# Optimization experiments

Hardware: AMD Instinct MI355X
Metric: run time of the kernel (lower is better)

## Reference

```python
import jax, jax.numpy as jnp
import numpy as np

DIM_V = 512
NUM_HEADS = 8
LN_EPS = 1e-5


def _layernorm(x):
    # LayerNorm over last dim, no affine (simplified_layer_norm=True)
    mu = jnp.mean(x, axis=-1, keepdims=True)
    var = jnp.mean(jnp.square(x - mu), axis=-1, keepdims=True)
    return (x - mu) * jax.lax.rsqrt(var + LN_EPS)


def setup_inputs() -> dict:
    key = jax.random.key(0)
    ks = jax.random.split(key, 12)
    B, Nq, Nk, dQ, dK, dV = 16, 1024, 1024, 512, 512, DIM_V
    s = 0.02
    return {
        "Q": jax.random.normal(ks[0], (B, Nq, dQ), jnp.float32),
        "K": jax.random.normal(ks[1], (B, Nk, dK), jnp.float32),
        "Wq": jax.random.normal(ks[2], (dQ, dV), jnp.float32) * s,
        "bq": jnp.zeros((dV,), jnp.float32),
        "Wk": jax.random.normal(ks[3], (dK, dV), jnp.float32) * s,
        "bk": jnp.zeros((dV,), jnp.float32),
        "Wv": jax.random.normal(ks[4], (dK, dV), jnp.float32) * s,
        "bv": jnp.zeros((dV,), jnp.float32),
        "Wo": jax.random.normal(ks[5], (dV, dV), jnp.float32) * s,
        "bo": jnp.zeros((dV,), jnp.float32),
    }


def reference(Q, K, Wq, bq, Wk, bk, Wv, bv, Wo, bo):
    H = NUM_HEADS
    dh = DIM_V // H
    q = Q @ Wq + bq            # [B, Nq, dV]
    k = K @ Wk + bk            # [B, Nk, dV]
    v = K @ Wv + bv            # [B, Nk, dV]
    B, Nq, _ = q.shape
    Nk = k.shape[1]
    qh = q.reshape(B, Nq, H, dh)
    kh = k.reshape(B, Nk, H, dh)
    vh = v.reshape(B, Nk, H, dh)
    # NOTE: faithful to source — scale by sqrt(dim_V), not sqrt(head_dim)
    scores = jnp.einsum('bqhd,bkhd->bhqk', qh, kh) / jnp.sqrt(jnp.asarray(DIM_V, q.dtype))
    A = jax.nn.softmax(scores, axis=-1)                    # [B, H, Nq, Nk]
    attn = jnp.einsum('bhqk,bkhd->bqhd', A, vh).reshape(B, Nq, DIM_V)
    O = q + attn               # residual with projected Q
    O = _layernorm(O)          # ln0 (no affine)
    O = O + jax.nn.gelu(O @ Wo + bo, approximate=False)
    O = _layernorm(O)          # ln1 (no affine)
    return O
```

## Files before the change

### kernel.cpp

```cpp
#include <hip/hip_runtime.h>
#include <hip/hip_bf16.h>
#include <math.h>

typedef __bf16 bf16;
typedef __bf16 bf16x8 __attribute__((ext_vector_type(8)));
typedef float  f32x4  __attribute__((ext_vector_type(4)));
typedef float  f32x16 __attribute__((ext_vector_type(16)));
typedef unsigned u32x4 __attribute__((ext_vector_type(4)));

#define MFMA16(a,b,c) __builtin_amdgcn_mfma_f32_16x16x32_bf16((a),(b),(c),0,0,0)
#define MFMA32(a,b,c) __builtin_amdgcn_mfma_f32_32x32x16_bf16((a),(b),(c),0,0,0)
#define KSCALE 0.0637587159f

__device__ __forceinline__ void async16p(const void* g, void* l) {
    __builtin_amdgcn_global_load_lds((const __attribute__((address_space(1))) void*)g,
                                     (__attribute__((address_space(3))) void*)l,
                                     16, 0, 0);
}

__device__ __forceinline__ float fexp2(float x) {
#if __has_builtin(__builtin_amdgcn_exp2f)
    return __builtin_amdgcn_exp2f(x);
#else
    return exp2f(x);
#endif
}

__device__ __forceinline__ unsigned pkbf(float a, float b) {
    union { bf16 h[2]; unsigned u; } x;
    x.h[0] = (bf16)a; x.h[1] = (bf16)b; return x.u;
}

__device__ __forceinline__ void plswap(unsigned &a, unsigned &b) {
#if __has_builtin(__builtin_amdgcn_permlane32_swap)
    auto r = __builtin_amdgcn_permlane32_swap((int)a, (int)b, false, false);
    a = (unsigned)r[0]; b = (unsigned)r[1];
#else
    unsigned sa = (unsigned)__shfl_xor((int)a, 32);
    unsigned sb = (unsigned)__shfl_xor((int)b, 32);
    bool hi = (threadIdx.x & 32) != 0;
    unsigned na = hi ? sb : a;
    unsigned nb = hi ? b  : sa;
    a = na; b = nb;
#endif
}

__global__ __launch_bounds__(256) void prep_w_kernel(
    const float* __restrict__ Wq, const float* __restrict__ Wk,
    const float* __restrict__ Wv, const float* __restrict__ Wo,
    bf16* __restrict__ WqT, bf16* __restrict__ WkT,
    bf16* __restrict__ WvT, bf16* __restrict__ WoT,
    float* __restrict__ csum)
{
    __shared__ float tile[32][33];
    const int bx = blockIdx.x;
    const float* W; bf16* T;
    switch (bx >> 8) {
      case 0: W=Wq; T=WqT; break;
      case 1: W=Wk; T=WkT; break;
      case 2: W=Wv; T=WvT; break;
      default: W=Wo; T=WoT; break;
    }
    const int rest = bx & 255;
    const int k0 = (rest & 15) * 32, n0 = (rest >> 4) * 32;
    const int tx = threadIdx.x & 31, ty = threadIdx.x >> 5;
    float sacc = 0.f;
    #pragma unroll
    for (int i=0;i<32;i+=8) {
        float v = W[(size_t)(k0+ty+i)*512 + n0+tx];
        tile[ty+i][tx] = v;
        sacc += v;
    }
    __syncthreads();
    #pragma unroll
    for (int i=0;i<32;i+=8)
        T[(size_t)(n0+ty+i)*512 + k0+tx] = (bf16)tile[tx][ty+i];
    if ((bx >> 8) == 3) {
        __syncthreads();
        tile[ty][tx] = sacc;
        __syncthreads();
        if (ty == 0) {
            float s = 0.f;
            #pragma unroll
            for (int j=0;j<8;j++) s += tile[j][tx];
            atomicAdd(&csum[n0+tx], s);
        }
    }
}

__global__ __launch_bounds__(256, 2) void gemm_proj_kernel(
    const float* __restrict__ Qf, const float* __restrict__ Kf,
    const bf16* __restrict__ WqT, const bf16* __restrict__ WkT,
    const bf16* __restrict__ WvT,
    const float* __restrict__ bq, const float* __restrict__ bk,
    const float* __restrict__ bv,
    bf16* __restrict__ qbb, bf16* __restrict__ kbb, bf16* __restrict__ vT)
{
    __shared__ __align__(16) char smem[65536];
    float* As32 = (float*)smem;
    bf16*  Bs   = (bf16*)(smem + 32768);
    bf16*  Lt   = (bf16*)smem;

    const int x = blockIdx.x;
    const bool isQ = (x < 256);
    int m0, n0;
    const float* A; const bf16 *BT0, *BT1; const float *bb0, *bb1;
    if (isQ) {
        const int n = (x >> 3) & 1;
        const int m = (x & 7) | ((x >> 4) << 3);
        m0 = m * 128; n0 = n * 128;
        A = Qf; BT0 = WqT + (size_t)n0*512; BT1 = WqT + (size_t)(n0+256)*512;
        bb0 = bq + n0; bb1 = bq + n0 + 256;
    } else {
        const int r = x - 256;
        const int n = (r >> 3) & 3;
        const int m = (r & 7) | ((r >> 5) << 3);
        m0 = m * 128; n0 = n * 128;
        A = Kf; BT0 = WkT + (size_t)n0*512; BT1 = WvT + (size_t)n0*512;
        bb0 = bk + n0; bb1 = bv + n0;
    }

    const int tid = threadIdx.x;
    const int lane = tid & 63, wave = tid >> 6;
    const int qd = lane >> 4, lr = lane & 15;
    const int wm = (wave & 1) * 64, wn = (wave >> 1) * 64;

    const float* gA = A + (size_t)(m0 + (tid>>3))*512 + (((tid&7)^((tid>>3)&7))*4);
    const int bgr = ((tid & 3) ^ ((tid >> 3) & 3)) * 8;
    const bf16* gB0 = BT0 + (size_t)(tid>>2)*512 + bgr;
    const bf16* gB1 = BT1 + (size_t)(tid>>2)*512 + bgr;

    f32x4 acc[2][4][4];
    #pragma unroll
    for (int p=0;p<2;p++)
      #pragma unroll
      for (int i=0;i<4;i++)
        #pragma unroll
        for (int j=0;j<4;j++) acc[p][i][j] = (f32x4){0,0,0,0};

    auto stage = [&](int buf, int k0) {
        float* lA = As32 + buf*4096 + wave*256;
        #pragma unroll
        for (int i=0;i<4;i++)
            async16p(gA + k0 + (size_t)i*32*512, lA + i*1024);
        bf16* lB0 = Bs + buf*8192 + wave*512;
        async16p(gB0 + k0,                  lB0);
        async16p(gB0 + k0 + (size_t)64*512, lB0 + 2048);
        bf16* lB1 = Bs + buf*8192 + 4096 + wave*512;
        async16p(gB1 + k0,                  lB1);
        async16p(gB1 + k0 + (size_t)64*512, lB1 + 2048);
    };

    stage(0, 0);
    for (int t = 0; t < 16; ++t) {
        const int cur = t & 1;
        __builtin_amdgcn_sched_barrier(0);
        __builtin_amdgcn_s_barrier();
        if (t < 15) {
            stage(cur ^ 1, (t+1)*32);
            asm volatile("s_waitcnt vmcnt(8)" ::: "memory");
        } else {
            asm volatile("s_waitcnt vmcnt(0)" ::: "memory");
        }
        __builtin_amdgcn_s_barrier();

        const float* Ab = As32 + cur*4096;
        const bf16*  Bb = Bs   + cur*8192;
        bf16x8 af[4], bfr[2][4];
        #pragma unroll
        for (int mi=0;mi<4;mi++) {
            int row = wm + mi*16 + lr;
            f32x4 f0 = *(f32x4*)(Ab + row*32 + (((qd*2  )^(lr&7))*4));
            f32x4 f1 = *(f32x4*)(Ab + row*32 + (((qd*2+1)^(lr&7))*4));
            bf16x8 a;
            a[0]=(bf16)f0[0]; a[1]=(bf16)f0[1]; a[2]=(bf16)f0[2]; a[3]=(bf16)f0[3];
            a[4]=(bf16)f1[0]; a[5]=(bf16)f1[1]; a[6]=(bf16)f1[2]; a[7]=(bf16)f1[3];
            af[mi] = a;
        }
        #pragma unroll
        for (int p=0;p<2;p++)
          #pragma unroll
          for (int ni=0;ni<4;ni++)
            bfr[p][ni] = *(bf16x8*)(Bb + p*4096 + (wn+ni*16+lr)*32
                                       + ((qd^((lr>>1)&3))*8));
        #pragma unroll
        for (int p=0;p<2;p++)
          #pragma unroll
          for (int mi=0;mi<4;mi++)
            #pragma unroll
            for (int ni=0;ni<4;ni++)
              acc[p][mi][ni] = MFMA16(af[mi], bfr[p][ni], acc[p][mi][ni]);
    }

    if (isQ) {
        #pragma unroll
        for (int p=0;p<2;p++) {
            const float* bb = p ? bb1 : bb0;
            #pragma unroll
            for (int ni=0;ni<4;ni++) {
                int nl = wn + ni*16 + lr;
                int n = n0 + p*256 + nl;
                float bv0 = bb[nl];
                #pragma unroll
                for (int mi=0;mi<4;mi++) {
                    int mb = m0 + wm + mi*16 + qd*4;
                    #pragma unroll
                    for (int r=0;r<4;r++)
                        qbb[(size_t)(mb+r)*512 + n] = (bf16)(acc[p][mi][ni][r] + bv0);
                }
            }
        }
    } else {
        #pragma unroll
        for (int ni=0;ni<4;ni++) {
            int nl = wn + ni*16 + lr;
            int n = n0 + nl;
            float bv0 = bb0[nl];
            #pragma unroll
            for (int mi=0;mi<4;mi++) {
                int mb = m0 + wm + mi*16 + qd*4;
                #pragma unroll
                for (int r=0;r<4;r++)
                    kbb[(size_t)(mb+r)*512 + n] = (bf16)((acc[0][mi][ni][r] + bv0)*KSCALE);
            }
        }
        const int b = m0 >> 10, tok0 = m0 & 1023;
        const int row = tid >> 2, ch = tid & 3;
        #pragma unroll
        for (int half = 0; half < 2; ++half) {
            __syncthreads();
            if ((wn >> 6) == half) {
                #pragma unroll
                for (int ni=0;ni<4;ni++) {
                    int nl = ni*16 + lr;
                    float bvv = bb1[half*64 + nl];
                    #pragma unroll
                    for (int mi=0;mi<4;mi++)
                      #pragma unroll
                      for (int r=0;r<4;r++) {
                        int col = wm + mi*16 + qd*4 + r;
                        Lt[nl*128 + ((((col>>3)^(nl&7))<<3) | (col&7))]
                            = (bf16)(acc[1][mi][ni][r] + bvv);
                      }
                }
            }
            __syncthreads();
            const int h = (n0 >> 6) + half;
            bf16* dst = vT + ((size_t)((b*8 + h)*64 + row))*1024 + tok0 + ch*32;
            #pragma unroll
            for (int s=0;s<4;s++) {
                int g = (ch*4 + s) ^ (row & 7);
                *(uint4*)(dst + s*8) = *(uint4*)(Lt + row*128 + g*8);
            }
        }
    }
}

__global__ __launch_bounds__(256, 4) void attn_kernel(
    const bf16* __restrict__ qb, const bf16* __restrict__ kb,
    const bf16* __restrict__ vT, bf16* __restrict__ attnb)
{
    const int x = blockIdx.x;
    const int qt = x >> 7, h = x & 7, b = (x & 127) >> 3;
    const int tid = threadIdx.x, lane = tid & 63, wave = tid >> 6;
    const int l = lane & 31, hi = lane >> 5;
    const int q0w = qt*128 + wave*32;

    __shared__ __align__(16) bf16 kv[2][2][4096];
    __shared__ float ls[4][32];

    bf16x8 aq[4];
    {
        const bf16* qrow = qb + ((size_t)(b*1024 + q0w + l))*512 + h*64 + hi*8;
        #pragma unroll
        for (int st=0; st<4; ++st) aq[st] = *(const bf16x8*)(qrow + st*16);
    }

    const int srow = lane >> 3;
    const int sgA  = (lane & 7) ^ srow ^ wave;
    const int sgB  = sgA ^ 4;
    const bf16* kg0 = kb + ((size_t)(b*1024 + wave*8 + srow))*512      + h*64 + sgA*8;
    const bf16* kg1 = kb + ((size_t)(b*1024 + wave*8 + srow + 32))*512 + h*64 + sgB*8;
    const bf16* vg0 = vT + ((size_t)((b*8 + h)*64 + wave*8 + srow))*1024      + sgA*8;
    const bf16* vg1 = vT + ((size_t)((b*8 + h)*64 + wave*8 + srow + 32))*1024 + sgB*8;

    auto stage = [&](int buf, int t) {
        const size_t ko = (size_t)t*64*512;
        async16p(kg0 + ko,     &kv[buf][0][wave*512]);
        async16p(kg1 + ko,     &kv[buf][0][2048 + wave*512]);
        async16p(vg0 + t*64,   &kv[buf][1][wave*512]);
        async16p(vg1 + t*64,   &kv[buf][1][2048 + wave*512]);
    };

    f32x16 accO[2];
    accO[0] = (f32x16)0.f; accO[1] = (f32x16)0.f;
    float lsum = 0.f;
    const int kx = (l & 7) ^ (l >> 3);

    stage(0, 0);
    for (int t=0; t<16; ++t) {
        const int cur = t & 1;
        __builtin_amdgcn_sched_barrier(0);
        __builtin_amdgcn_s_barrier();
        if (t < 15) {
            stage(cur ^ 1, t + 1);
            asm volatile("s_waitcnt vmcnt(4)" ::: "memory");
        } else {
            asm volatile("s_waitcnt vmcnt(0)" ::: "memory");
        }
        __builtin_amdgcn_s_barrier();

        const bf16* Ks = kv[cur][0];
        const bf16* Vs = kv[cur][1];

        u32x4 paf[4];
        #pragma unroll
        for (int kb2=0; kb2<2; ++kb2) {
            f32x16 sT = (f32x16)0.f;
            __builtin_amdgcn_s_setprio(1);
            #pragma unroll
            for (int st=0; st<4; ++st) {
                bf16x8 kf = *(const bf16x8*)(Ks + (kb2*32 + l)*64
                               + (((st*2 + hi) ^ kx ^ (kb2<<2))*8));
                sT = MFMA32(kf, aq[st], sT);
            }
            __builtin_amdgcn_s_setprio(0);
            unsigned u[8];
            #pragma unroll
            for (int m=0; m<8; ++m) {
                float e0 = fexp2(sT[2*m]);
                float e1 = fexp2(sT[2*m+1]);
                lsum += e0 + e1;
                u[m] = pkbf(e0, e1);
            }
            #pragma unroll
            for (int sb=0; sb<2; ++sb) {
                unsigned a0=u[4*sb], a1=u[4*sb+1], a2=u[4*sb+2], a3=u[4*sb+3];
                plswap(a0, a2);
                plswap(a1, a3);
                paf[kb2*2 + sb] = (u32x4){a0, a1, a2, a3};
            }
        }
        __builtin_amdgcn_s_setprio(1);
        #pragma unroll
        for (int db=0; db<2; ++db) {
            f32x16 a = accO[db];
            #pragma unroll
            for (int st=0; st<4; ++st) {
                bf16x8 vf = *(const bf16x8*)(Vs + (db*32 + l)*64
                               + (((st*2 + hi) ^ kx ^ (db<<2))*8));
                u32x4 pp = paf[st];
                bf16x8 pf = *(bf16x8*)&pp;
                a = MFMA32(pf, vf, a);
            }
            accO[db] = a;
        }
        __builtin_amdgcn_s_setprio(0);
    }

    lsum += __shfl_xor(lsum, 32);
    ls[wave][l] = lsum;
    __syncthreads();

    #pragma unroll
    for (int g=0; g<4; ++g) {
        f32x4 lv = *(const f32x4*)(&ls[wave][g*8 + hi*4]);
        f32x4 inv;
        #pragma unroll
        for (int i=0;i<4;i++) inv[i] = 1.f / lv[i];
        #pragma unroll
        for (int db=0; db<2; ++db) {
            #pragma unroll
            for (int i=0;i<4;i++) {
                int r = g*4 + i;
                int qrow = q0w + g*8 + hi*4 + i;
                size_t idx = ((size_t)(b*1024 + qrow))*512 + h*64 + db*32 + l;
                float o = accO[db][r] * inv[i] + (float)qb[idx];
                attnb[idx] = (bf16)o;
            }
        }
    }
}

__global__ __launch_bounds__(256, 4) void gemm_o_kernel(
    const bf16* __restrict__ attnb, const bf16* __restrict__ WoT,
    const float* __restrict__ bo, const float* __restrict__ csum,
    bf16* __restrict__ xb)
{
    __shared__ __align__(16) char smem[24576];
    __shared__ float2 rs[64];
    bf16* As = (bf16*)smem;
    bf16* Bs = (bf16*)(smem + 8192);
    const int m0 = blockIdx.x * 64, n0 = blockIdx.y * 128;
    const int tid = threadIdx.x;
    const int lane = tid & 63, wave = tid >> 6;
    const int qd = lane >> 4, lr = lane & 15;
    const int wm = (wave & 1) * 32, wn = (wave >> 1) * 64;

    const int bgr = ((tid & 3) ^ ((tid >> 3) & 3)) * 8;
    const bf16* gA = attnb + (size_t)(m0 + (tid>>2))*512 + bgr;
    const bf16* gB = WoT   + (size_t)(n0 + (tid>>2))*512 + bgr;

    f32x4 acc[2][4];
    #pragma unroll
    for (int i=0;i<2;i++)
      #pragma unroll
      for (int j=0;j<4;j++) acc[i][j] = (f32x4){0,0,0,0};
    float s1[2] = {0.f, 0.f}, s2[2] = {0.f, 0.f};

    auto stage = [&](int buf, int k0) {
        async16p(gA + k0,                  As + buf*2048 + wave*512);
        bf16* lB = Bs + buf*4096 + wave*512;
        async16p(gB + k0,                  lB);
        async16p(gB + k0 + (size_t)64*512, lB + 2048);
    };

    stage(0, 0);
    for (int t = 0; t < 16; ++t) {
        const int cur = t & 1;
        __builtin_amdgcn_sched_barrier(0);
        __builtin_amdgcn_s_barrier();
        if (t < 15) {
            stage(cur ^ 1, (t+1)*32);
            asm volatile("s_waitcnt vmcnt(3)" ::: "memory");
        } else {
            asm volatile("s_waitcnt vmcnt(0)" ::: "memory");
        }
        __builtin_amdgcn_s_barrier();

        const bf16* Ab = As + cur*2048;
        const bf16* Bb = Bs + cur*4096;
        bf16x8 af[2], bfr[4];
        #pragma unroll
        for (int mi=0;mi<2;mi++) {
            af[mi] = *(bf16x8*)(Ab + (wm+mi*16+lr)*32 + ((qd^((lr>>1)&3))*8));
            #pragma unroll
            for (int j=0;j<8;j++) {
                float v = (float)af[mi][j];
                s1[mi] += v;
                s2[mi] += v*v;
            }
        }
        #pragma unroll
        for (int ni=0;ni<4;ni++)
            bfr[ni] = *(bf16x8*)(Bb + (wn+ni*16+lr)*32 + ((qd^((lr>>1)&3))*8));
        #pragma unroll
        for (int mi=0;mi<2;mi++)
          #pragma unroll
          for (int ni=0;ni<4;ni++)
            acc[mi][ni] = MFMA16(af[mi], bfr[ni], acc[mi][ni]);
    }

    #pragma unroll
    for (int mi=0;mi<2;mi++) {
        s1[mi] += __shfl_xor(s1[mi], 16); s2[mi] += __shfl_xor(s2[mi], 16);
        s1[mi] += __shfl_xor(s1[mi], 32); s2[mi] += __shfl_xor(s2[mi], 32);
    }
    if (wave < 2 && qd == 0) {
        #pragma unroll
        for (int mi=0;mi<2;mi++) {
            float mu  = s1[mi] * (1.f/512.f);
            float var = s2[mi] * (1.f/512.f) - mu*mu;
            rs[wm + mi*16 + lr] = make_float2(mu, rsqrtf(var + 1e-5f));
        }
    }
    __syncthreads();

    float csn[4], bon[4];
    #pragma unroll
    for (int ni=0;ni<4;ni++) {
        int n = n0 + wn + ni*16 + lr;
        csn[ni] = csum[n];
        bon[ni] = bo[n];
    }
    #pragma unroll
    for (int mi=0;mi<2;mi++) {
        #pragma unroll
        for (int r=0;r<4;r++) {
            int rl = wm + mi*16 + qd*4 + r;
            int row = m0 + rl;
            float2 st = rs[rl];
            float mu = st.x, rstd = st.y;
            #pragma unroll
            for (int ni=0;ni<4;ni++) {
                int n = n0 + wn + ni*16 + lr;
                float g = rstd*acc[mi][ni][r] - rstd*mu*csn[ni] + bon[ni];
                float gelu = 0.5f * g * (1.f + erff(g * 0.70710678118654752f));
                size_t idx = (size_t)row*512 + n;
                float lnx = ((float)attnb[idx] - mu) * rstd;
                xb[idx] = (bf16)(lnx + gelu);
            }
        }
    }
}

__global__ __launch_bounds__(256) void ln1_kernel(
    const bf16* __restrict__ xb, float* __restrict__ out)
{
    const int wave = threadIdx.x >> 6, lane = threadIdx.x & 63;
    const int row = blockIdx.x*4 + wave;
    const size_t base = (size_t)row*512 + lane*8;
    bf16x8 xv = *(const bf16x8*)(xb + base);
    float x[8];
    #pragma unroll
    for (int i=0;i<8;i++) x[i] = (float)xv[i];
    float s1 = 0.f, s2 = 0.f;
    #pragma unroll
    for (int i=0;i<8;i++){ s1 += x[i]; s2 += x[i]*x[i]; }
    #pragma unroll
    for (int off=1; off<64; off<<=1) { s1 += __shfl_xor(s1, off); s2 += __shfl_xor(s2, off); }
    float mu  = s1 * (1.f/512.f);
    float var = s2 * (1.f/512.f) - mu*mu;
    float rstd = rsqrtf(var + 1e-5f);
    float4 o0 = {(x[0]-mu)*rstd,(x[1]-mu)*rstd,(x[2]-mu)*rstd,(x[3]-mu)*rstd};
    float4 o1 = {(x[4]-mu)*rstd,(x[5]-mu)*rstd,(x[6]-mu)*rstd,(x[7]-mu)*rstd};
    *(float4*)(out + base)     = o0;
    *(float4*)(out + base + 4) = o1;
}

extern "C" void kernel_launch(void* const* d_in, const int* in_sizes, int n_in,
                              void* d_out, int out_size, void* d_ws, size_t ws_size,
                              hipStream_t stream)
{
    (void)in_sizes; (void)n_in; (void)out_size; (void)ws_size;
    const float* Q  = (const float*)d_in[0];
    const float* K  = (const float*)d_in[1];
    const float* Wq = (const float*)d_in[2];
    const float* bq = (const float*)d_in[3];
    const float* Wk = (const float*)d_in[4];
    const float* bk = (const float*)d_in[5];
    const float* Wv = (const float*)d_in[6];
    const float* bv = (const float*)d_in[7];
    const float* Wo = (const float*)d_in[8];
    const float* bo = (const float*)d_in[9];
    float* out = (float*)d_out;

    const size_t nTok = (size_t)16*1024*512;
    char* p = (char*)d_ws;
    auto alloc = [&](size_t bytes)->char* {
        char* r = p; p += (bytes + 255) & ~(size_t)255; return r;
    };
    bf16*   WqT   = (bf16*)alloc(512*512*2);
    bf16*   WkT   = (bf16*)alloc(512*512*2);
    bf16*   WvT   = (bf16*)alloc(512*512*2);
    bf16*   WoT   = (bf16*)alloc(512*512*2);
    bf16*   qbb   = (bf16*)alloc(nTok*2);
    bf16*   kbb   = (bf16*)alloc(nTok*2);
    bf16*   vT    = (bf16*)alloc(nTok*2);
    bf16*   attnb = (bf16*)alloc(nTok*2);
    bf16*   xb    = (bf16*)alloc(nTok*2);
    float*  csum  = (float*)alloc(512*4);

    hipMemsetAsync(csum, 0, 512*sizeof(float), stream);
    prep_w_kernel<<<1024, 256, 0, stream>>>(Wq, Wk, Wv, Wo, WqT, WkT, WvT, WoT, csum);
    gemm_proj_kernel<<<768, 256, 0, stream>>>(Q, K, WqT, WkT, WvT,
                                              bq, bk, bv, qbb, kbb, vT);
    attn_kernel<<<dim3(1024), 256, 0, stream>>>(qbb, kbb, vT, attnb);
    gemm_o_kernel<<<dim3(256,4), 256, 0, stream>>>(attnb, WoT, bo, csum, xb);
    ln1_kernel<<<4096, 256, 0, stream>>>(xb, out);
}
```

Baseline: 243.5 us.

## Convert projection A tile to bf16 in registers before LDS; drop csum atomics

The projection GEMM no longer async-copies fp32 A tiles into LDS and converts them at fragment-load time. It now loads fp32 A into registers two stages ahead, packs it to bf16, and writes a swizzled bf16 tile to LDS. This shrinks LDS from 64KB to 48KB and halves A's LDS read traffic, at the cost of extra registers and explicit waitcnt choreography. Separately, the Wo column-sum atomics and the memset are replaced by per-block partial sums that gemm_o reduces over 16 entries.

```diff
diff --git a/kernel.cpp b/kernel.cpp
--- a/kernel.cpp
+++ b/kernel.cpp
@@ -50,7 +50,7 @@
     const float* __restrict__ Wv, const float* __restrict__ Wo,
     bf16* __restrict__ WqT, bf16* __restrict__ WkT,
     bf16* __restrict__ WvT, bf16* __restrict__ WoT,
-    float* __restrict__ csum)
+    float* __restrict__ csump)
 {
     __shared__ float tile[32][33];
     const int bx = blockIdx.x;
@@ -83,7 +83,7 @@
             float s = 0.f;
             #pragma unroll
             for (int j=0;j<8;j++) s += tile[j][tx];
-            atomicAdd(&csum[n0+tx], s);
+            csump[(rest & 15)*512 + n0 + tx] = s;
         }
     }
 }
@@ -96,10 +96,10 @@
     const float* __restrict__ bv,
     bf16* __restrict__ qbb, bf16* __restrict__ kbb, bf16* __restrict__ vT)
 {
-    __shared__ __align__(16) char smem[65536];
-    float* As32 = (float*)smem;
-    bf16*  Bs   = (bf16*)(smem + 32768);
-    bf16*  Lt   = (bf16*)smem;
+    __shared__ __align__(16) char smem[49152];
+    bf16* Asb = (bf16*)smem;
+    bf16* Bs  = (bf16*)(smem + 16384);
+    bf16* Lt  = (bf16*)smem;
 
     const int x = blockIdx.x;
     const bool isQ = (x < 256);
@@ -125,7 +125,13 @@
     const int qd = lane >> 4, lr = lane & 15;
     const int wm = (wave & 1) * 64, wn = (wave >> 1) * 64;
 
-    const float* gA = A + (size_t)(m0 + (tid>>3))*512 + (((tid&7)^((tid>>3)&7))*4);
+    const int arow = tid >> 1, ahalf = tid & 1;
+    const float* gAr = A + (size_t)(m0 + arow)*512 + ahalf*16;
+    const int akey = (arow >> 1) & 3;
+    const int ap0 = (2*ahalf) ^ akey;
+    const int ap1 = ap0 ^ 1;
+    bf16* awr = Asb + arow*32;
+
     const int bgr = ((tid & 3) ^ ((tid >> 3) & 3)) * 8;
     const bf16* gB0 = BT0 + (size_t)(tid>>2)*512 + bgr;
     const bf16* gB1 = BT1 + (size_t)(tid>>2)*512 + bgr;
@@ -138,11 +144,7 @@
         #pragma unroll
         for (int j=0;j<4;j++) acc[p][i][j] = (f32x4){0,0,0,0};
 
-    auto stage = [&](int buf, int k0) {
-        float* lA = As32 + buf*4096 + wave*256;
-        #pragma unroll
-        for (int i=0;i<4;i++)
-            async16p(gA + k0 + (size_t)i*32*512, lA + i*1024);
+    auto stageB = [&](int buf, int k0) {
         bf16* lB0 = Bs + buf*8192 + wave*512;
         async16p(gB0 + k0,                  lB0);
         async16p(gB0 + k0 + (size_t)64*512, lB0 + 2048);
@@ -150,33 +152,27 @@
         async16p(gB1 + k0,                  lB1);
         async16p(gB1 + k0 + (size_t)64*512, lB1 + 2048);
     };
-
-    stage(0, 0);
-    for (int t = 0; t < 16; ++t) {
-        const int cur = t & 1;
-        __builtin_amdgcn_sched_barrier(0);
-        __builtin_amdgcn_s_barrier();
-        if (t < 15) {
-            stage(cur ^ 1, (t+1)*32);
-            asm volatile("s_waitcnt vmcnt(8)" ::: "memory");
-        } else {
-            asm volatile("s_waitcnt vmcnt(0)" ::: "memory");
-        }
-        __builtin_amdgcn_s_barrier();
-
-        const float* Ab = As32 + cur*4096;
-        const bf16*  Bb = Bs   + cur*8192;
+    auto loadA = [&](f32x4 (&ar)[4], int k0) {
+        ar[0] = *(const f32x4*)(gAr + k0);
+        ar[1] = *(const f32x4*)(gAr + k0 + 4);
+        ar[2] = *(const f32x4*)(gAr + k0 + 8);
+        ar[3] = *(const f32x4*)(gAr + k0 + 12);
+    };
+    auto writeA = [&](f32x4 (&ar)[4], int buf) {
+        u32x4 w0 = { pkbf(ar[0][0],ar[0][1]), pkbf(ar[0][2],ar[0][3]),
+                     pkbf(ar[1][0],ar[1][1]), pkbf(ar[1][2],ar[1][3]) };
+        u32x4 w1 = { pkbf(ar[2][0],ar[2][1]), pkbf(ar[2][2],ar[2][3]),
+                     pkbf(ar[3][0],ar[3][1]), pkbf(ar[3][2],ar[3][3]) };
+        *(u32x4*)(awr + buf*4096 + ap0*8) = w0;
+        *(u32x4*)(awr + buf*4096 + ap1*8) = w1;
+    };
+    auto compute = [&](int cur) {
+        const bf16* Ab = Asb + cur*4096;
+        const bf16* Bb = Bs  + cur*8192;
         bf16x8 af[4], bfr[2][4];
         #pragma unroll
-        for (int mi=0;mi<4;mi++) {
-            int row = wm + mi*16 + lr;
-            f32x4 f0 = *(f32x4*)(Ab + row*32 + (((qd*2  )^(lr&7))*4));
-            f32x4 f1 = *(f32x4*)(Ab + row*32 + (((qd*2+1)^(lr&7))*4));
-            bf16x8 a;
-            a[0]=(bf16)f0[0]; a[1]=(bf16)f0[1]; a[2]=(bf16)f0[2]; a[3]=(bf16)f0[3];
-            a[4]=(bf16)f1[0]; a[5]=(bf16)f1[1]; a[6]=(bf16)f1[2]; a[7]=(bf16)f1[3];
-            af[mi] = a;
-        }
+        for (int mi=0;mi<4;mi++)
+            af[mi] = *(bf16x8*)(Ab + (wm+mi*16+lr)*32 + ((qd ^ ((lr>>1)&3))*8));
         #pragma unroll
         for (int p=0;p<2;p++)
           #pragma unroll
@@ -190,6 +186,47 @@
             #pragma unroll
             for (int ni=0;ni<4;ni++)
               acc[p][mi][ni] = MFMA16(af[mi], bfr[p][ni], acc[p][mi][ni]);
+    };
+
+    f32x4 aR0[4], aR1[4];
+    loadA(aR0, 0);
+    asm volatile("s_waitcnt vmcnt(0)" ::: "memory");
+    writeA(aR0, 0);
+    loadA(aR0, 32);
+    stageB(0, 0);
+    asm volatile("s_waitcnt lgkmcnt(0)" ::: "memory");
+
+    auto phase = [&](int t, f32x4 (&aWr)[4], f32x4 (&aLd)[4]) {
+        __builtin_amdgcn_sched_barrier(0);
+        __builtin_amdgcn_s_barrier();
+        loadA(aLd, (t+2)*32);
+        stageB((t+1)&1, (t+1)*32);
+        asm volatile("s_waitcnt vmcnt(8)" ::: "memory");
+        writeA(aWr, (t+1)&1);
+        asm volatile("s_waitcnt lgkmcnt(0)" ::: "memory");
+        __builtin_amdgcn_s_barrier();
+        compute(t & 1);
+    };
+
+    #pragma unroll 1
+    for (int tt = 0; tt < 7; ++tt) {
+        phase(2*tt,   aR0, aR1);
+        phase(2*tt+1, aR1, aR0);
+    }
+    {
+        __builtin_amdgcn_sched_barrier(0);
+        __builtin_amdgcn_s_barrier();
+        stageB(1, 480);
+        asm volatile("s_waitcnt vmcnt(4)" ::: "memory");
+        writeA(aR0, 1);
+        asm volatile("s_waitcnt lgkmcnt(0)" ::: "memory");
+        __builtin_amdgcn_s_barrier();
+        compute(0);
+    }
+    {
+        asm volatile("s_waitcnt vmcnt(0)" ::: "memory");
+        __builtin_amdgcn_s_barrier();
+        compute(1);
     }
 
     if (isQ) {
@@ -384,7 +421,7 @@
 
 __global__ __launch_bounds__(256, 4) void gemm_o_kernel(
     const bf16* __restrict__ attnb, const bf16* __restrict__ WoT,
-    const float* __restrict__ bo, const float* __restrict__ csum,
+    const float* __restrict__ bo, const float* __restrict__ csump,
     bf16* __restrict__ xb)
 {
     __shared__ __align__(16) char smem[24576];
@@ -470,7 +507,10 @@
     #pragma unroll
     for (int ni=0;ni<4;ni++) {
         int n = n0 + wn + ni*16 + lr;
-        csn[ni] = csum[n];
+        float s = 0.f;
+        #pragma unroll
+        for (int kb=0;kb<16;kb++) s += csump[kb*512 + n];
+        csn[ni] = s;
         bon[ni] = bo[n];
     }
     #pragma unroll
@@ -549,13 +589,12 @@
     bf16*   vT    = (bf16*)alloc(nTok*2);
     bf16*   attnb = (bf16*)alloc(nTok*2);
     bf16*   xb    = (bf16*)alloc(nTok*2);
-    float*  csum  = (float*)alloc(512*4);
-
-    hipMemsetAsync(csum, 0, 512*sizeof(float), stream);
-    prep_w_kernel<<<1024, 256, 0, stream>>>(Wq, Wk, Wv, Wo, WqT, WkT, WvT, WoT, csum);
+    float*  csump = (float*)alloc(16*512*4);
+
+    prep_w_kernel<<<1024, 256, 0, stream>>>(Wq, Wk, Wv, Wo, WqT, WkT, WvT, WoT, csump);
     gemm_proj_kernel<<<768, 256, 0, stream>>>(Q, K, WqT, WkT, WvT,
                                               bq, bk, bv, qbb, kbb, vT);
     attn_kernel<<<dim3(1024), 256, 0, stream>>>(qbb, kbb, vT, attnb);
-    gemm_o_kernel<<<dim3(256,4), 256, 0, stream>>>(attnb, WoT, bo, csum, xb);
+    gemm_o_kernel<<<dim3(256,4), 256, 0, stream>>>(attnb, WoT, bo, csump, xb);
     ln1_kernel<<<4096, 256, 0, stream>>>(xb, out);
 }
```

Result: slower. 250.5 us (+2.9%).
